# Performance work log

Hardware: AMD Instinct MI355X
Metric: run time of the kernel (lower is better)

## Reference

```python
import jax, jax.numpy as jnp
import numpy as np

# Static problem sizes (must match setup_inputs)
B = 4                 # batch (scenes)
N_POINTS = 524288     # total points across batch (data_dict['feats'].shape[0])
NUM_PROPOSAL = 256    # fixed slots per scene (self.num_proposal)
FEAT_DIM = 16         # hard-coded in torch.zeros(..., 16)


def setup_inputs() -> dict:
    key = jax.random.key(0)
    k1, k2, k3 = jax.random.split(key, 3)
    P = 256            # total proposals across batch
    PPB = P // B       # proposals per scene = 64 (< NUM_PROPOSAL -> no topk branch)
    PTS_PER_BATCH = N_POINTS // B
    PPP = 4096         # points per proposal
    M = P * PPP
    K_INST = 32        # max GT instances per scene (ious second dim)

    rng = np.random.RandomState(0)
    pid = np.repeat(np.arange(P), PPP)                     # (M,) proposal id, sorted
    bat = pid // PPB                                       # scene of each entry
    ptid = rng.randint(0, PTS_PER_BATCH, size=M) + bat * PTS_PER_BATCH
    proposals_idx = np.stack([pid, ptid], axis=1).astype(np.int64)   # (M, 2)
    proposals_offset = (np.arange(P + 1) * PPP).astype(np.int64)     # (P+1,)
    batch_offsets = (np.arange(B + 1) * PTS_PER_BATCH).astype(np.int64)  # (B+1,)

    return {
        "scores": jax.random.normal(k1, (P, 1), dtype=jnp.float32),
        "score_feats": jax.random.normal(k2, (P, FEAT_DIM), dtype=jnp.float32),
        "ious": jax.random.uniform(k3, (P, K_INST), dtype=jnp.float32),
        "proposals_idx": jnp.asarray(proposals_idx),
        "proposals_offset": jnp.asarray(proposals_offset),
        "batch_offsets": jnp.asarray(batch_offsets),
    }


def reference(scores, score_feats, ious, proposals_idx, proposals_offset, batch_offsets):
    P = score_feats.shape[0]

    # scores_pred = sigmoid(scores.view(-1))
    scores_pred = jax.nn.sigmoid(scores.reshape(-1))                      # (P,)

    # proposals_pred[pid, ptid] = 1  -- big irregular scatter, (P, N) int32
    proposals_pred = jnp.zeros((P, N_POINTS), dtype=jnp.int32)
    proposals_pred = proposals_pred.at[proposals_idx[:, 0], proposals_idx[:, 1]].set(1)

    # batch index of each proposal from the first point in the proposal
    # (equivalent to the python boundary-search loop over batch_offsets)
    first_pt = proposals_idx[proposals_offset[:-1], 1]                    # (P,)
    b_idx = jnp.searchsorted(batch_offsets, first_pt, side="right") - 1   # (P,) in [0,B)

    # slot of each proposal within its scene (rank of appearance, loop order)
    onehot = jax.nn.one_hot(b_idx, B, dtype=jnp.int32)                    # (P, B)
    slot = jnp.cumsum(onehot, axis=0)[jnp.arange(P), b_idx] - 1           # (P,)

    # pack into fixed-size per-scene tensors (topk overflow branch not taken:
    # per-scene count <= NUM_PROPOSAL by construction, matching common path)
    batch = jnp.zeros((B, NUM_PROPOSAL, FEAT_DIM), dtype=score_feats.dtype)
    batch = batch.at[b_idx, slot].set(score_feats)

    proposal_mask = jnp.zeros((B, NUM_PROPOSAL), dtype=jnp.float32)
    proposal_mask = proposal_mask.at[b_idx, slot].set(1.0)

    K_INST = ious.shape[1]
    proposal_ious = jnp.zeros((B, NUM_PROPOSAL, K_INST), dtype=ious.dtype)
    proposal_ious = proposal_ious.at[b_idx, slot].set(ious)

    return batch, proposal_mask, scores_pred, proposal_ious, proposals_pred
```

## Files before the change

### kernel.cpp

```cpp
#include <hip/hip_runtime.h>


#define N_POINTS_C 524288
#define NUM_PROPOSAL_C 256
#define FEAT_DIM_C 16
#define SPLIT 2
#define HALF_WORDS (N_POINTS_C / 32 / SPLIT)

__global__ void proposal_small_kernel(const float* __restrict__ scores,
                                      const float* __restrict__ feats,
                                      const float* __restrict__ ious,
                                      const int* __restrict__ pidx,
                                      const int* __restrict__ poff,
                                      const int* __restrict__ boff,
                                      int P, int nB, int K,
                                      float* __restrict__ out_batch,
                                      float* __restrict__ out_mask,
                                      float* __restrict__ out_spred,
                                      float* __restrict__ out_ious) {
    __shared__ int sb[NUM_PROPOSAL_C];
    const int p = threadIdx.x;

    {
        const int nbatch = nB * NUM_PROPOSAL_C * FEAT_DIM_C;
        for (int i = p; i < nbatch; i += blockDim.x) out_batch[i] = 0.0f;
        const int nmask = nB * NUM_PROPOSAL_C;
        for (int i = p; i < nmask; i += blockDim.x) out_mask[i] = 0.0f;
        const int nious = nB * NUM_PROPOSAL_C * K;
        for (int i = p; i < nious; i += blockDim.x) out_ious[i] = 0.0f;
    }

    int b = 0;
    if (p < P) {
        const int fp = pidx[2 * poff[p] + 1];
        b = nB - 1;
        for (int j = 0; j < nB; ++j) {
            if (fp < boff[j + 1]) { b = j; break; }
        }
        sb[p] = b;
    }
    __syncthreads();
    if (p < P) {
        int slot = 0;
        for (int q = 0; q < p; ++q) slot += (sb[q] == b) ? 1 : 0;

        out_mask[b * NUM_PROPOSAL_C + slot] = 1.0f;
        out_spred[p] = 1.0f / (1.0f + expf(-scores[p]));

        const int dst_bs = b * NUM_PROPOSAL_C + slot;
        #pragma unroll
        for (int j = 0; j < FEAT_DIM_C; ++j)
            out_batch[dst_bs * FEAT_DIM_C + j] = feats[p * FEAT_DIM_C + j];
        for (int j = 0; j < K; ++j)
            out_ious[dst_bs * K + j] = ious[p * K + j];
    }
}

__global__ __launch_bounds__(1024, 2)
void proposals_pred_kernel(const int* __restrict__ pidx,
                           const int* __restrict__ poff,
                           float* __restrict__ out_pp) {
    __shared__ unsigned bm[HALF_WORDS];
    const int p    = blockIdx.x / SPLIT;
    const int part = blockIdx.x % SPLIT;
    const int tid  = threadIdx.x;
    const int lo   = part * (N_POINTS_C / SPLIT);
    const int hi   = lo + (N_POINTS_C / SPLIT);

    #pragma unroll
    for (int w = tid; w < HALF_WORDS; w += 1024) bm[w] = 0u;
    __syncthreads();

    const int s = poff[p];
    const int e = poff[p + 1];
    for (int i = s + tid; i < e; i += 1024) {
        const int pt = pidx[2 * i + 1];
        if (pt >= lo && pt < hi) {
            const int rel = pt - lo;
            atomicOr(&bm[rel >> 5], 1u << (rel & 31));
        }
    }
    __syncthreads();

    float4* dst = (float4*)(out_pp + (size_t)p * N_POINTS_C + lo);
    const int nvec = (N_POINTS_C / SPLIT) / 4;
    #pragma unroll 4
    for (int v = tid; v < nvec; v += 1024) {
        const unsigned w = bm[v >> 3];
        const int sh = (v & 7) * 4;
        float4 o;
        o.x = ((w >> (sh + 0)) & 1u) ? 1.0f : 0.0f;
        o.y = ((w >> (sh + 1)) & 1u) ? 1.0f : 0.0f;
        o.z = ((w >> (sh + 2)) & 1u) ? 1.0f : 0.0f;
        o.w = ((w >> (sh + 3)) & 1u) ? 1.0f : 0.0f;
        dst[v] = o;
    }
}

extern "C" void kernel_launch(void* const* d_in, const int* in_sizes, int n_in,
                              void* d_out, int out_size, void* d_ws, size_t ws_size,
                              hipStream_t stream) {
    const float* scores = (const float*)d_in[0];
    const float* feats  = (const float*)d_in[1];
    const float* ious   = (const float*)d_in[2];
    const int*   pidx   = (const int*)d_in[3];
    const int*   poff   = (const int*)d_in[4];
    const int*   boff   = (const int*)d_in[5];

    const int P  = in_sizes[0];
    const int K  = in_sizes[2] / P;
    const int nB = in_sizes[5] - 1;

    float* out = (float*)d_out;
    float* out_batch = out;
    float* out_mask  = out_batch + (size_t)nB * NUM_PROPOSAL_C * FEAT_DIM_C;
    float* out_spred = out_mask  + (size_t)nB * NUM_PROPOSAL_C;
    float* out_ious  = out_spred + P;
    float* out_pp    = out_ious  + (size_t)nB * NUM_PROPOSAL_C * K;

    proposal_small_kernel<<<1, 256, 0, stream>>>(scores, feats, ious, pidx,
                                                 poff, boff, P, nB, K,
                                                 out_batch, out_mask,
                                                 out_spred, out_ious);

    proposals_pred_kernel<<<P * SPLIT, 1024, 0, stream>>>(pidx, poff, out_pp);
}
```

Before: 551.3 us.

## Fuse small packing kernel into proposals scatter kernel, vectorize index loads, nontemporal stores

Merges the single-block packing kernel into the big bitmap-scatter kernel as an extra block, removing one launch and its serialization. Index pairs are now read two at a time via int4 loads, halving the load instructions. The dense output is written with nontemporal stores so the large write stream does not pollute cache. The extra block's shared array is reused for the slot computation, and it relies on the int4 loads being 16-byte aligned.

New measurement: 531.6 us. 1.04x faster.

```diff
diff --git a/kernel.cpp b/kernel.cpp
--- a/kernel.cpp
+++ b/kernel.cpp
@@ -7,63 +7,64 @@
 #define SPLIT 2
 #define HALF_WORDS (N_POINTS_C / 32 / SPLIT)
 
-__global__ void proposal_small_kernel(const float* __restrict__ scores,
-                                      const float* __restrict__ feats,
-                                      const float* __restrict__ ious,
-                                      const int* __restrict__ pidx,
-                                      const int* __restrict__ poff,
-                                      const int* __restrict__ boff,
-                                      int P, int nB, int K,
-                                      float* __restrict__ out_batch,
-                                      float* __restrict__ out_mask,
-                                      float* __restrict__ out_spred,
-                                      float* __restrict__ out_ious) {
-    __shared__ int sb[NUM_PROPOSAL_C];
-    const int p = threadIdx.x;
+typedef float vfloat4 __attribute__((ext_vector_type(4)));
 
-    {
+__global__ __launch_bounds__(1024, 2)
+void fused_kernel(const float* __restrict__ scores,
+                  const float* __restrict__ feats,
+                  const float* __restrict__ ious,
+                  const int* __restrict__ pidx,
+                  const int* __restrict__ poff,
+                  const int* __restrict__ boff,
+                  int P, int nB, int K,
+                  float* __restrict__ out_batch,
+                  float* __restrict__ out_mask,
+                  float* __restrict__ out_spred,
+                  float* __restrict__ out_ious,
+                  float* __restrict__ out_pp) {
+    __shared__ unsigned bm[HALF_WORDS];
+    const int tid = threadIdx.x;
+
+    if (blockIdx.x == (unsigned)(P * SPLIT)) {
+        int* sb = (int*)bm;
+
         const int nbatch = nB * NUM_PROPOSAL_C * FEAT_DIM_C;
-        for (int i = p; i < nbatch; i += blockDim.x) out_batch[i] = 0.0f;
+        for (int i = tid; i < nbatch; i += blockDim.x) out_batch[i] = 0.0f;
         const int nmask = nB * NUM_PROPOSAL_C;
-        for (int i = p; i < nmask; i += blockDim.x) out_mask[i] = 0.0f;
+        for (int i = tid; i < nmask; i += blockDim.x) out_mask[i] = 0.0f;
         const int nious = nB * NUM_PROPOSAL_C * K;
-        for (int i = p; i < nious; i += blockDim.x) out_ious[i] = 0.0f;
+        for (int i = tid; i < nious; i += blockDim.x) out_ious[i] = 0.0f;
+
+        const int p = tid;
+        int b = 0;
+        if (p < P) {
+            const int fp = pidx[2 * poff[p] + 1];
+            b = nB - 1;
+            for (int j = 0; j < nB; ++j) {
+                if (fp < boff[j + 1]) { b = j; break; }
+            }
+            sb[p] = b;
+        }
+        __syncthreads();
+        if (p < P) {
+            int slot = 0;
+            for (int q = 0; q < p; ++q) slot += (sb[q] == b) ? 1 : 0;
+
+            out_mask[b * NUM_PROPOSAL_C + slot] = 1.0f;
+            out_spred[p] = 1.0f / (1.0f + expf(-scores[p]));
+
+            const int dst_bs = b * NUM_PROPOSAL_C + slot;
+            #pragma unroll
+            for (int j = 0; j < FEAT_DIM_C; ++j)
+                out_batch[dst_bs * FEAT_DIM_C + j] = feats[p * FEAT_DIM_C + j];
+            for (int j = 0; j < K; ++j)
+                out_ious[dst_bs * K + j] = ious[p * K + j];
+        }
+        return;
     }
 
-    int b = 0;
-    if (p < P) {
-        const int fp = pidx[2 * poff[p] + 1];
-        b = nB - 1;
-        for (int j = 0; j < nB; ++j) {
-            if (fp < boff[j + 1]) { b = j; break; }
-        }
-        sb[p] = b;
-    }
-    __syncthreads();
-    if (p < P) {
-        int slot = 0;
-        for (int q = 0; q < p; ++q) slot += (sb[q] == b) ? 1 : 0;
-
-        out_mask[b * NUM_PROPOSAL_C + slot] = 1.0f;
-        out_spred[p] = 1.0f / (1.0f + expf(-scores[p]));
-
-        const int dst_bs = b * NUM_PROPOSAL_C + slot;
-        #pragma unroll
-        for (int j = 0; j < FEAT_DIM_C; ++j)
-            out_batch[dst_bs * FEAT_DIM_C + j] = feats[p * FEAT_DIM_C + j];
-        for (int j = 0; j < K; ++j)
-            out_ious[dst_bs * K + j] = ious[p * K + j];
-    }
-}
-
-__global__ __launch_bounds__(1024, 2)
-void proposals_pred_kernel(const int* __restrict__ pidx,
-                           const int* __restrict__ poff,
-                           float* __restrict__ out_pp) {
-    __shared__ unsigned bm[HALF_WORDS];
     const int p    = blockIdx.x / SPLIT;
     const int part = blockIdx.x % SPLIT;
-    const int tid  = threadIdx.x;
     const int lo   = part * (N_POINTS_C / SPLIT);
     const int hi   = lo + (N_POINTS_C / SPLIT);
 
@@ -71,29 +72,46 @@
     for (int w = tid; w < HALF_WORDS; w += 1024) bm[w] = 0u;
     __syncthreads();
 
-    const int s = poff[p];
-    const int e = poff[p + 1];
-    for (int i = s + tid; i < e; i += 1024) {
-        const int pt = pidx[2 * i + 1];
-        if (pt >= lo && pt < hi) {
-            const int rel = pt - lo;
-            atomicOr(&bm[rel >> 5], 1u << (rel & 31));
+    {
+        const int s = poff[p];
+        const int e = poff[p + 1];
+        const int4* pp4 = (const int4*)(pidx + 2 * s);
+        const int npair2 = (e - s) / 2;
+        for (int i = tid; i < npair2; i += 1024) {
+            const int4 q = pp4[i];
+            if (q.y >= lo && q.y < hi) {
+                const int rel = q.y - lo;
+                atomicOr(&bm[rel >> 5], 1u << (rel & 31));
+            }
+            if (q.w >= lo && q.w < hi) {
+                const int rel = q.w - lo;
+                atomicOr(&bm[rel >> 5], 1u << (rel & 31));
+            }
+        }
+        if ((e - s) & 1) {
+            if (tid == 0) {
+                const int pt = pidx[2 * (e - 1) + 1];
+                if (pt >= lo && pt < hi) {
+                    const int rel = pt - lo;
+                    atomicOr(&bm[rel >> 5], 1u << (rel & 31));
+                }
+            }
         }
     }
     __syncthreads();
 
-    float4* dst = (float4*)(out_pp + (size_t)p * N_POINTS_C + lo);
+    vfloat4* dst = (vfloat4*)(out_pp + (size_t)p * N_POINTS_C + lo);
     const int nvec = (N_POINTS_C / SPLIT) / 4;
     #pragma unroll 4
     for (int v = tid; v < nvec; v += 1024) {
         const unsigned w = bm[v >> 3];
         const int sh = (v & 7) * 4;
-        float4 o;
+        vfloat4 o;
         o.x = ((w >> (sh + 0)) & 1u) ? 1.0f : 0.0f;
         o.y = ((w >> (sh + 1)) & 1u) ? 1.0f : 0.0f;
         o.z = ((w >> (sh + 2)) & 1u) ? 1.0f : 0.0f;
         o.w = ((w >> (sh + 3)) & 1u) ? 1.0f : 0.0f;
-        dst[v] = o;
+        __builtin_nontemporal_store(o, &dst[v]);
     }
 }
 
@@ -118,10 +136,9 @@
     float* out_ious  = out_spred + P;
     float* out_pp    = out_ious  + (size_t)nB * NUM_PROPOSAL_C * K;
 
-    proposal_small_kernel<<<1, 256, 0, stream>>>(scores, feats, ious, pidx,
-                                                 poff, boff, P, nB, K,
-                                                 out_batch, out_mask,
-                                                 out_spred, out_ious);
-
-    proposals_pred_kernel<<<P * SPLIT, 1024, 0, stream>>>(pidx, poff, out_pp);
+    fused_kernel<<<P * SPLIT + 1, 1024, 0, stream>>>(scores, feats, ious, pidx,
+                                                     poff, boff, P, nB, K,
+                                                     out_batch, out_mask,
+                                                     out_spred, out_ious,
+                                                     out_pp);
 }
```
